# Optimization experiments

Measured on AMD Instinct MI355X. Metric: run time of the kernel, lower is better.

## Reference

```python
import jax, jax.numpy as jnp
import numpy as np

DECAY = 0.99
EPS = 1e-05


def setup_inputs() -> dict:
    key = jax.random.key(0)
    k1, k2 = jax.random.split(key)
    B, C, H, W = 16, 64, 32, 32
    K = 8192
    z_e = jax.random.normal(k1, (B, C, H, W), dtype=jnp.float32)
    embedding = jax.random.normal(k2, (K, C), dtype=jnp.float32)
    cluster_size = jnp.zeros((K,), dtype=jnp.float32)
    embedding_avg = embedding  # initialized as a clone of the codebook
    return {"z_e": z_e, "embedding": embedding, "cluster_size": cluster_size,
            "embedding_avg": embedding_avg}


def reference(z_e, embedding, cluster_size, embedding_avg):
    B, C, H, W = z_e.shape
    K = embedding.shape[0]
    # [N, C] tokens
    z_flat = jnp.transpose(z_e, (0, 2, 3, 1)).reshape(-1, C)
    d = ((z_flat * z_flat).sum(-1, keepdims=True)
         - 2.0 * (z_flat @ embedding.T)
         + (embedding * embedding).sum(-1))
    indices = jnp.argmin(d, axis=1)  # [N] int
    z_q_flat = embedding[indices]    # [N, C]
    z_q = jnp.transpose(z_q_flat.reshape(B, H, W, C), (0, 3, 1, 2))
    # EMA codebook update (training path); one-hot matmuls expressed as segment sums
    counts = jax.ops.segment_sum(jnp.ones(z_flat.shape[0], dtype=z_flat.dtype),
                                 indices, num_segments=K)            # encodings.sum(0)
    dw = jax.ops.segment_sum(z_flat, indices, num_segments=K)        # encodings.T @ z_flat
    new_cluster_size = DECAY * cluster_size + (1.0 - DECAY) * counts
    new_embedding_avg = DECAY * embedding_avg + (1.0 - DECAY) * dw
    n = new_cluster_size.sum()
    cs = (new_cluster_size + EPS) / (n + K * EPS) * n
    new_embedding = new_embedding_avg / cs[:, None]
    # straight-through estimator
    z_q_st = z_e + jax.lax.stop_gradient(z_q - z_e)
    return (z_q_st, indices.reshape(B, H * W), z_q,
            new_embedding, new_cluster_size, new_embedding_avg)
```

## Files before the change

kernel.cpp:

```cpp
#include <hip/hip_runtime.h>

#define DECAYF 0.99f
#define OMDF   0.01f
#define TAU    3.5e-2f

typedef unsigned int u32;
typedef unsigned long long u64;
typedef __attribute__((ext_vector_type(8))) _Float16 f16x8;
typedef __attribute__((ext_vector_type(4))) float f32x4;

#define EN_OFF     0
#define EFRAG_OFF  32768
#define IDX_OFF    32768
#define BEST1_OFF  2129920
#define BEST2_OFF  4227072
#define CNT_OFF    5275648

__device__ __forceinline__ u64 enc_pair(float s, int idx) {
  u32 u = __float_as_uint(s);
  u = (u & 0x80000000u) ? ~u : (u | 0x80000000u);
  return ((u64)u << 32) | (u32)(~idx);
}
__device__ __forceinline__ float dec_score(u64 e) {
  u32 u = (u32)(e >> 32);
  u = (u & 0x80000000u) ? (u & 0x7fffffffu) : ~u;
  return __uint_as_float(u);
}
__device__ __forceinline__ int dec_idx(u64 e) { return (int)(~(u32)e); }
__device__ __forceinline__ unsigned short f2h(float f) {
  union { _Float16 h; unsigned short u; } v;
  v.h = (_Float16)f;
  return v.u;
}
__device__ __forceinline__ float exact_dot(const float* __restrict__ sx,
                                           const float* __restrict__ emb, int k) {
  const float4* e = (const float4*)(emb + (size_t)k * 64);
  float a = 0.f;
#pragma unroll
  for (int q = 0; q < 16; ++q) {
    float4 v = e[q];
    a = fmaf(sx[4 * q],     v.x, a);
    a = fmaf(sx[4 * q + 1], v.y, a);
    a = fmaf(sx[4 * q + 2], v.z, a);
    a = fmaf(sx[4 * q + 3], v.w, a);
  }
  return a;
}

__global__ __launch_bounds__(256) void k_prep(const float* __restrict__ emb,
                                              const float* __restrict__ cs_in,
                                              const float* __restrict__ avg_in,
                                              const float* __restrict__ z_e,
                                              float* __restrict__ en,
                                              unsigned char* __restrict__ efrag,
                                              unsigned char* __restrict__ zfrag,
                                              float* __restrict__ out4,
                                              float* __restrict__ out5,
                                              float* __restrict__ nsum) {
  __shared__ float warr[4];
  __shared__ float sx[64][129];
  int bid = blockIdx.x;
  int t = threadIdx.x;
  if (bid < 512) {
    int tid = bid * 256 + t;
    int k = tid >> 4, q = tid & 15;
    float4 v = ((const float4*)emb)[tid];
    ushort4 hv;
    hv.x = f2h(v.x); hv.y = f2h(v.y); hv.z = f2h(v.z); hv.w = f2h(v.w);
    size_t off = (size_t)(k >> 4) * 2048 + (size_t)(q >> 3) * 1024
               + (size_t)((q >> 1) & 3) * 256 + (size_t)(k & 15) * 16
               + (size_t)(q & 1) * 8;
    *(ushort4*)(efrag + off) = hv;
    float s = v.x * v.x + v.y * v.y + v.z * v.z + v.w * v.w;
    s += __shfl_xor(s, 1, 16);
    s += __shfl_xor(s, 2, 16);
    s += __shfl_xor(s, 4, 16);
    s += __shfl_xor(s, 8, 16);
    if (q == 0) en[k] = 0.5f * s;
  } else if (bid < 1031) {
    int tid = (bid - 512) * 256 + t;
    if (tid < 131072) {
      float4 v = ((const float4*)avg_in)[tid];
      v.x *= DECAYF; v.y *= DECAYF; v.z *= DECAYF; v.w *= DECAYF;
      ((float4*)out5)[tid] = v;
    }
  } else if (bid == 1031) {
    float s = 0.f;
#pragma unroll
    for (int q = 0; q < 8; ++q) {
      int idx = q * 256 + t;
      float4 v = ((const float4*)cs_in)[idx];
      v.x *= DECAYF; v.y *= DECAYF; v.z *= DECAYF; v.w *= DECAYF;
      ((float4*)out4)[idx] = v;
      s += v.x + v.y + v.z + v.w;
    }
    s += __shfl_xor(s, 1, 64);
    s += __shfl_xor(s, 2, 64);
    s += __shfl_xor(s, 4, 64);
    s += __shfl_xor(s, 8, 64);
    s += __shfl_xor(s, 16, 64);
    s += __shfl_xor(s, 32, 64);
    if ((t & 63) == 0) warr[t >> 6] = s;
    __syncthreads();
    if (t == 0) *nsum = warr[0] + warr[1] + warr[2] + warr[3];
  } else {
    int n0 = (bid - 1032) * 128;
    int b = n0 >> 10, hwb = n0 & 1023;
#pragma unroll
    for (int r = 0; r < 8; ++r) {
      int g = r * 256 + t;
      int c = g >> 5, f4 = g & 31;
      float4 v = *(const float4*)(z_e + ((size_t)b << 16) + ((size_t)c << 10)
                                  + hwb + f4 * 4);
      sx[c][f4 * 4 + 0] = v.x;
      sx[c][f4 * 4 + 1] = v.y;
      sx[c][f4 * 4 + 2] = v.z;
      sx[c][f4 * 4 + 3] = v.w;
    }
    __syncthreads();
#pragma unroll
    for (int r = 0; r < 4; ++r) {
      int id = r * 256 + t;
      int nl = id & 127, k = id >> 7;
      int n = n0 + nl;
      unsigned short u[8];
#pragma unroll
      for (int j = 0; j < 8; ++j) u[j] = f2h(sx[k * 8 + j][nl]);
      size_t off = (size_t)(n >> 4) * 2048 + (size_t)(k >> 2) * 1024
                 + (size_t)(k & 3) * 256 + (size_t)(n & 15) * 16;
      *(ushort4*)(zfrag + off)     = make_ushort4(u[0], u[1], u[2], u[3]);
      *(ushort4*)(zfrag + off + 8) = make_ushort4(u[4], u[5], u[6], u[7]);
    }
  }
}

__global__ __launch_bounds__(256) void k_argmin_mfma(
    const unsigned char* __restrict__ zfrag,
    const unsigned char* __restrict__ efrag,
    const float* __restrict__ en, u64* __restrict__ best1,
    float* __restrict__ best2) {
  alignas(16) __shared__ unsigned char sbuf[2][8192];
  __shared__ float sen[512];
  const int tb = blockIdx.x >> 4;
  const int sl = blockIdx.x & 15;
  const int wave = threadIdx.x >> 6, lane = threadIdx.x & 63;
  const int col = lane & 15, g4 = lane >> 4;
  const int token0 = tb * 128 + wave * 32;
  const int scb = sl << 9;

  if (threadIdx.x < 128)
    ((float4*)sen)[threadIdx.x] = ((const float4*)(en + scb))[threadIdx.x];

  f16x8 a[2][2];
  {
    const unsigned char* zb = zfrag + ((size_t)(tb * 8 + wave * 2)) * 2048
                            + (size_t)g4 * 256 + (size_t)col * 16;
    a[0][0] = *(const f16x8*)(zb);
    a[0][1] = *(const f16x8*)(zb + 1024);
    a[1][0] = *(const f16x8*)(zb + 2048);
    a[1][1] = *(const f16x8*)(zb + 3072);
  }
  float b1[8], b2[8];
#pragma unroll
  for (int r = 0; r < 8; ++r) { b1[r] = -3.0e38f; b2[r] = -3.0e38f; }

  const unsigned char* gbase0 = efrag + (size_t)scb * 128;
  auto stage = [&](int ib, int buf) {
    const unsigned char* g = gbase0 + (size_t)ib * 8192 + (size_t)wave * 2048;
#pragma unroll
    for (int it = 0; it < 2; ++it) {
      __builtin_amdgcn_global_load_lds(
          (const __attribute__((address_space(1))) u32*)(g + it * 1024 + lane * 16),
          (__attribute__((address_space(3))) u32*)(&sbuf[buf][wave * 2048 + it * 1024]),
          16, 0, 0);
    }
  };
  stage(0, 0);
  for (int ib = 0; ib < 8; ++ib) {
    __syncthreads();
    if (ib < 7) stage(ib + 1, (ib + 1) & 1);
    const unsigned char* sb0 = &sbuf[ib & 1][0];
#pragma unroll
    for (int ct = 0; ct < 4; ++ct) {
      const int t = ib * 4 + ct;
      const float negen = -sen[t * 16 + col];
      f16x8 bf0 = *(const f16x8*)(sb0 + ct * 2048 + lane * 16);
      f16x8 bf1 = *(const f16x8*)(sb0 + ct * 2048 + 1024 + lane * 16);
      f32x4 acc0, acc1;
#pragma unroll
      for (int r = 0; r < 4; ++r) { acc0[r] = negen; acc1[r] = negen; }
      acc0 = __builtin_amdgcn_mfma_f32_16x16x32_f16(a[0][0], bf0, acc0, 0, 0, 0);
      acc0 = __builtin_amdgcn_mfma_f32_16x16x32_f16(a[0][1], bf1, acc0, 0, 0, 0);
      acc1 = __builtin_amdgcn_mfma_f32_16x16x32_f16(a[1][0], bf0, acc1, 0, 0, 0);
      acc1 = __builtin_amdgcn_mfma_f32_16x16x32_f16(a[1][1], bf1, acc1, 0, 0, 0);
      const u32 emb6 = (u32)(63 - t);
#pragma unroll
      for (int r = 0; r < 4; ++r) {
        float f0 = __uint_as_float((__float_as_uint(acc0[r]) & 0xFFFFFFC0u) | emb6);
        b2[r] = __builtin_amdgcn_fmed3f(f0, b1[r], b2[r]);
        b1[r] = fmaxf(b1[r], f0);
        float f1 = __uint_as_float((__float_as_uint(acc1[r]) & 0xFFFFFFC0u) | emb6);
        b2[4 + r] = __builtin_amdgcn_fmed3f(f1, b1[4 + r], b2[4 + r]);
        b1[4 + r] = fmaxf(b1[4 + r], f1);
      }
    }
  }
  int mi[8];
#pragma unroll
  for (int r = 0; r < 8; ++r) mi[r] = col;
#pragma unroll
  for (int st = 1; st < 16; st <<= 1) {
#pragma unroll
    for (int r = 0; r < 8; ++r) {
      float ob1 = __shfl_xor(b1[r], st, 64);
      float ob2 = __shfl_xor(b2[r], st, 64);
      int omi = __shfl_xor(mi[r], st, 64);
      bool ogt = ob1 > b1[r];
      b2[r] = fmaxf(fminf(b1[r], ob1), fmaxf(b2[r], ob2));
      mi[r] = ogt ? omi : mi[r];
      b1[r] = fmaxf(b1[r], ob1);
    }
  }
  if (col == 0) {
#pragma unroll
    for (int r = 0; r < 8; ++r) {
      int tt = r >> 2, rr = r & 3;
      int token = token0 + tt * 16 + g4 * 4 + rr;
      int t = 63 - (int)(__float_as_uint(b1[r]) & 63u);
      int gcode = scb + t * 16 + mi[r];
      best1[(size_t)sl * 16384 + token] = enc_pair(b1[r], gcode);
      best2[(size_t)sl * 16384 + token] = b2[r];
    }
  }
}

__global__ __launch_bounds__(256) void k_resfix(const float* __restrict__ z_e,
                                                const float* __restrict__ emb,
                                                const float* __restrict__ en,
                                                const u64* __restrict__ best1,
                                                const float* __restrict__ best2,
                                                int* __restrict__ idxa) {
  __shared__ float sxr[64];
  __shared__ int flist[64];
  __shared__ float fth[64];
  __shared__ int nflag;
  __shared__ u32 fmask;
  __shared__ u64 red;
  int t = threadIdx.x;
  int n0 = blockIdx.x * 64;
  if (t == 0) nflag = 0;
  __syncthreads();
  if (t < 64) {
    int n = n0 + t;
    u64 e[16];
#pragma unroll
    for (int s = 0; s < 16; ++s) e[s] = best1[(size_t)s * 16384 + n];
    u64 top = e[0];
#pragma unroll
    for (int s = 1; s < 16; ++s) top = e[s] > top ? e[s] : top;
    float second = -3.0e38f;
#pragma unroll
    for (int s = 0; s < 16; ++s)
      second = fmaxf(second, best2[(size_t)s * 16384 + n]);
#pragma unroll
    for (int s = 0; s < 16; ++s)
      if (e[s] != top) second = fmaxf(second, dec_score(e[s]));
    idxa[n] = dec_idx(top);
    if (dec_score(top) - second < TAU) {
      int p = atomicAdd(&nflag, 1);
      flist[p] = n;
      fth[p] = dec_score(top);
    }
  }
  __syncthreads();
  int nf = nflag;
  for (int i = 0; i < nf; ++i) {
    int n = flist[i];
    float theta = fth[i] - TAU;
    if (t == 0) { fmask = 0; red = 0ull; }
    if (t < 64) {
      sxr[t] = z_e[((size_t)(n >> 10) << 16) + ((size_t)t << 10) + (n & 1023)];
    }
    __syncthreads();
    u64 myb = 0ull;
    if (t < 16) {
      u64 es = best1[(size_t)t * 16384 + n];
      if (best2[(size_t)t * 16384 + n] >= theta) atomicOr(&fmask, 1u << t);
      if (dec_score(es) >= theta) {
        int k = dec_idx(es);
        float a = exact_dot(sxr, emb, k) - en[k];
        myb = enc_pair(a, k);
      }
    }
    __syncthreads();
    u32 fm = fmask;
    while (fm) {
      int s = __ffs(fm) - 1;
      fm &= fm - 1;
      int k0 = (s << 9) + t;
      float a0 = exact_dot(sxr, emb, k0)       - en[k0];
      float a1 = exact_dot(sxr, emb, k0 + 256) - en[k0 + 256];
      u64 m0 = enc_pair(a0, k0), m1 = enc_pair(a1, k0 + 256);
      u64 mm = m0 > m1 ? m0 : m1;
      myb = mm > myb ? mm : myb;
    }
    if (myb) atomicMax(&red, myb);
    __syncthreads();
    if (t == 0) idxa[n] = dec_idx(red);
    __syncthreads();
  }
}

__global__ __launch_bounds__(256) void k_scatter(const float* __restrict__ z_e,
                                                 const int* __restrict__ idxa,
                                                 float* __restrict__ out4,
                                                 float* __restrict__ out5) {
  __shared__ float sx[64][129];
  int t = threadIdx.x;
  int n0 = blockIdx.x * 128;
  int b = n0 >> 10, hwb = n0 & 1023;
#pragma unroll
  for (int r = 0; r < 8; ++r) {
    int g = r * 256 + t;
    int c = g >> 5, f4 = g & 31;
    float4 v = *(const float4*)(z_e + ((size_t)b << 16) + ((size_t)c << 10)
                                + hwb + f4 * 4);
    sx[c][f4 * 4 + 0] = v.x;
    sx[c][f4 * 4 + 1] = v.y;
    sx[c][f4 * 4 + 2] = v.z;
    sx[c][f4 * 4 + 3] = v.w;
  }
  __syncthreads();
  int wave = t >> 6, lane = t & 63;
#pragma unroll
  for (int i = 0; i < 32; ++i) {
    int tok = wave * 32 + i;
    int idx = idxa[n0 + tok];
    atomicAdd(out5 + (size_t)idx * 64 + lane, OMDF * sx[lane][tok]);
    if (lane == 0) atomicAdd(out4 + idx, OMDF);
  }
}

__global__ __launch_bounds__(256) void k_gather(const float* __restrict__ z_e,
                                                const float* __restrict__ emb,
                                                const int* __restrict__ idxa,
                                                float* __restrict__ out0,
                                                float* __restrict__ out1,
                                                float* __restrict__ out2) {
  int tid = blockIdx.x * 256 + threadIdx.x;
  int hw4 = tid & 255;
  int c   = (tid >> 8) & 63;
  int b   = tid >> 14;
  int n0  = (b << 10) + (hw4 << 2);
  size_t off = ((size_t)b << 16) + ((size_t)c << 10) + ((size_t)hw4 << 2);
  float4 z = *(const float4*)(z_e + off);
  int i0 = idxa[n0], i1 = idxa[n0 + 1], i2 = idxa[n0 + 2], i3 = idxa[n0 + 3];
  float4 q;
  q.x = emb[(size_t)i0 * 64 + c];
  q.y = emb[(size_t)i1 * 64 + c];
  q.z = emb[(size_t)i2 * 64 + c];
  q.w = emb[(size_t)i3 * 64 + c];
  float4 st;
  st.x = z.x + (q.x - z.x);
  st.y = z.y + (q.y - z.y);
  st.z = z.z + (q.z - z.z);
  st.w = z.w + (q.w - z.w);
  *(float4*)(out2 + off) = q;
  *(float4*)(out0 + off) = st;
  if (c == 0) {
    float4 f = make_float4((float)i0, (float)i1, (float)i2, (float)i3);
    *(float4*)(out1 + n0) = f;
  }
}

__global__ __launch_bounds__(256) void k_final(const float* __restrict__ out4,
                                               const float* __restrict__ out5,
                                               const float* __restrict__ nsum,
                                               float* __restrict__ out3) {
  int tid = blockIdx.x * 256 + threadIdx.x;
  int k = tid >> 4;
  double nn  = (double)*nsum + 163.84;
  double ncs = (double)out4[k];
  double cs  = (ncs + 1e-5) / (nn + 8192.0 * 1e-5) * nn;
  float inv  = (float)(1.0 / cs);
  float4 v = ((const float4*)out5)[tid];
  v.x *= inv; v.y *= inv; v.z *= inv; v.w *= inv;
  ((float4*)out3)[tid] = v;
}

extern "C" void kernel_launch(void* const* d_in, const int* in_sizes, int n_in,
                              void* d_out, int out_size, void* d_ws, size_t ws_size,
                              hipStream_t stream) {
  const float* z_e    = (const float*)d_in[0];
  const float* emb    = (const float*)d_in[1];
  const float* cs_in  = (const float*)d_in[2];
  const float* avg_in = (const float*)d_in[3];

  float* out  = (float*)d_out;
  float* out0 = out;
  float* out1 = out0 + 1048576;
  float* out2 = out1 + 16384;
  float* out3 = out2 + 1048576;
  float* out4 = out3 + 524288;
  float* out5 = out4 + 8192;

  char* ws = (char*)d_ws;
  float* en            = (float*)(ws + EN_OFF);
  unsigned char* efrag = (unsigned char*)(ws + EFRAG_OFF);
  u64* best1           = (u64*)(ws + BEST1_OFF);
  float* best2         = (float*)(ws + BEST2_OFF);
  int* idxa            = (int*)(ws + IDX_OFF);
  float* nsum          = (float*)(ws + CNT_OFF + 4);
  unsigned char* zfrag = (unsigned char*)out0;

  k_prep       <<<1160, 256, 0, stream>>>(emb, cs_in, avg_in, z_e, en, efrag,
                                          zfrag, out4, out5, nsum);
  k_argmin_mfma<<<2048, 256, 0, stream>>>(zfrag, efrag, en, best1, best2);
  k_resfix     <<<256,  256, 0, stream>>>(z_e, emb, en, best1, best2, idxa);
  k_scatter    <<<128,  256, 0, stream>>>(z_e, idxa, out4, out5);
  k_gather     <<<1024, 256, 0, stream>>>(z_e, emb, idxa, out0, out1, out2);
  k_final      <<<512,  256, 0, stream>>>(out4, out5, nsum, out3);
}
```

Before: 151.5 us.

## Replace atomic scatter with counting-sort segment sums; retile argmin to 64 tokens

The float-atomic scatter of token vectors into the codebook average is replaced by a histogram, a prefix-scan kernel and a fill kernel that build per-code token lists. The gather kernel then sums each code's tokens directly, and the final kernel folds in the counts. Separately, the MFMA argmin kernel is retiled to 64 tokens by 1024 codes per block with 8 code slices instead of 16, which halves the partial-result traffic read by the fixup kernel. The cost is two extra launches, a single-block scan, and uncoalesced per-token reads of z_e in the segment sums.

```diff
diff --git a/kernel.cpp b/kernel.cpp
--- a/kernel.cpp
+++ b/kernel.cpp
@@ -12,9 +12,13 @@
 #define EN_OFF     0
 #define EFRAG_OFF  32768
 #define IDX_OFF    32768
+#define CNT8K_OFF  1081344
+#define OFFS_OFF   1114112
+#define FILLP_OFF  1146880
+#define TOKL_OFF   1179648
 #define BEST1_OFF  2129920
-#define BEST2_OFF  4227072
-#define CNT_OFF    5275648
+#define BEST2_OFF  3178496
+#define NSUM_OFF   3702784
 
 __device__ __forceinline__ u64 enc_pair(float s, int idx) {
   u32 u = __float_as_uint(s);
@@ -56,7 +60,8 @@
                                               unsigned char* __restrict__ zfrag,
                                               float* __restrict__ out4,
                                               float* __restrict__ out5,
-                                              float* __restrict__ nsum) {
+                                              float* __restrict__ nsum,
+                                              int* __restrict__ cnt8k) {
   __shared__ float warr[4];
   __shared__ float sx[64][129];
   int bid = blockIdx.x;
@@ -93,6 +98,7 @@
       v.x *= DECAYF; v.y *= DECAYF; v.z *= DECAYF; v.w *= DECAYF;
       ((float4*)out4)[idx] = v;
       s += v.x + v.y + v.z + v.w;
+      ((int4*)cnt8k)[idx] = make_int4(0, 0, 0, 0);
     }
     s += __shfl_xor(s, 1, 64);
     s += __shfl_xor(s, 2, 64);
@@ -140,29 +146,26 @@
     const float* __restrict__ en, u64* __restrict__ best1,
     float* __restrict__ best2) {
   alignas(16) __shared__ unsigned char sbuf[2][8192];
-  __shared__ float sen[512];
-  const int tb = blockIdx.x >> 4;
-  const int sl = blockIdx.x & 15;
+  __shared__ float sen[1024];
+  const int tb = blockIdx.x >> 3;
+  const int sl = blockIdx.x & 7;
   const int wave = threadIdx.x >> 6, lane = threadIdx.x & 63;
   const int col = lane & 15, g4 = lane >> 4;
-  const int token0 = tb * 128 + wave * 32;
-  const int scb = sl << 9;
-
-  if (threadIdx.x < 128)
-    ((float4*)sen)[threadIdx.x] = ((const float4*)(en + scb))[threadIdx.x];
-
-  f16x8 a[2][2];
+  const int token0 = tb * 64 + wave * 16;
+  const int scb = sl << 10;
+
+  ((float4*)sen)[threadIdx.x] = ((const float4*)(en + scb))[threadIdx.x];
+
+  f16x8 a0, a1;
   {
-    const unsigned char* zb = zfrag + ((size_t)(tb * 8 + wave * 2)) * 2048
+    const unsigned char* zb = zfrag + ((size_t)(tb * 4 + wave)) * 2048
                             + (size_t)g4 * 256 + (size_t)col * 16;
-    a[0][0] = *(const f16x8*)(zb);
-    a[0][1] = *(const f16x8*)(zb + 1024);
-    a[1][0] = *(const f16x8*)(zb + 2048);
-    a[1][1] = *(const f16x8*)(zb + 3072);
-  }
-  float b1[8], b2[8];
-#pragma unroll
-  for (int r = 0; r < 8; ++r) { b1[r] = -3.0e38f; b2[r] = -3.0e38f; }
+    a0 = *(const f16x8*)(zb);
+    a1 = *(const f16x8*)(zb + 1024);
+  }
+  float b1[4], b2[4];
+#pragma unroll
+  for (int r = 0; r < 4; ++r) { b1[r] = -3.0e38f; b2[r] = -3.0e38f; }
 
   const unsigned char* gbase0 = efrag + (size_t)scb * 128;
   auto stage = [&](int ib, int buf) {
@@ -176,9 +179,9 @@
     }
   };
   stage(0, 0);
-  for (int ib = 0; ib < 8; ++ib) {
-    __syncthreads();
-    if (ib < 7) stage(ib + 1, (ib + 1) & 1);
+  for (int ib = 0; ib < 16; ++ib) {
+    __syncthreads();
+    if (ib < 15) stage(ib + 1, (ib + 1) & 1);
     const unsigned char* sb0 = &sbuf[ib & 1][0];
 #pragma unroll
     for (int ct = 0; ct < 4; ++ct) {
@@ -186,32 +189,27 @@
       const float negen = -sen[t * 16 + col];
       f16x8 bf0 = *(const f16x8*)(sb0 + ct * 2048 + lane * 16);
       f16x8 bf1 = *(const f16x8*)(sb0 + ct * 2048 + 1024 + lane * 16);
-      f32x4 acc0, acc1;
-#pragma unroll
-      for (int r = 0; r < 4; ++r) { acc0[r] = negen; acc1[r] = negen; }
-      acc0 = __builtin_amdgcn_mfma_f32_16x16x32_f16(a[0][0], bf0, acc0, 0, 0, 0);
-      acc0 = __builtin_amdgcn_mfma_f32_16x16x32_f16(a[0][1], bf1, acc0, 0, 0, 0);
-      acc1 = __builtin_amdgcn_mfma_f32_16x16x32_f16(a[1][0], bf0, acc1, 0, 0, 0);
-      acc1 = __builtin_amdgcn_mfma_f32_16x16x32_f16(a[1][1], bf1, acc1, 0, 0, 0);
+      f32x4 acc;
+#pragma unroll
+      for (int r = 0; r < 4; ++r) acc[r] = negen;
+      acc = __builtin_amdgcn_mfma_f32_16x16x32_f16(a0, bf0, acc, 0, 0, 0);
+      acc = __builtin_amdgcn_mfma_f32_16x16x32_f16(a1, bf1, acc, 0, 0, 0);
       const u32 emb6 = (u32)(63 - t);
 #pragma unroll
       for (int r = 0; r < 4; ++r) {
-        float f0 = __uint_as_float((__float_as_uint(acc0[r]) & 0xFFFFFFC0u) | emb6);
+        float f0 = __uint_as_float((__float_as_uint(acc[r]) & 0xFFFFFFC0u) | emb6);
         b2[r] = __builtin_amdgcn_fmed3f(f0, b1[r], b2[r]);
         b1[r] = fmaxf(b1[r], f0);
-        float f1 = __uint_as_float((__float_as_uint(acc1[r]) & 0xFFFFFFC0u) | emb6);
-        b2[4 + r] = __builtin_amdgcn_fmed3f(f1, b1[4 + r], b2[4 + r]);
-        b1[4 + r] = fmaxf(b1[4 + r], f1);
       }
     }
   }
-  int mi[8];
-#pragma unroll
-  for (int r = 0; r < 8; ++r) mi[r] = col;
+  int mi[4];
+#pragma unroll
+  for (int r = 0; r < 4; ++r) mi[r] = col;
 #pragma unroll
   for (int st = 1; st < 16; st <<= 1) {
 #pragma unroll
-    for (int r = 0; r < 8; ++r) {
+    for (int r = 0; r < 4; ++r) {
       float ob1 = __shfl_xor(b1[r], st, 64);
       float ob2 = __shfl_xor(b2[r], st, 64);
       int omi = __shfl_xor(mi[r], st, 64);
@@ -223,9 +221,8 @@
   }
   if (col == 0) {
 #pragma unroll
-    for (int r = 0; r < 8; ++r) {
-      int tt = r >> 2, rr = r & 3;
-      int token = token0 + tt * 16 + g4 * 4 + rr;
+    for (int r = 0; r < 4; ++r) {
+      int token = token0 + g4 * 4 + r;
       int t = 63 - (int)(__float_as_uint(b1[r]) & 63u);
       int gcode = scb + t * 16 + mi[r];
       best1[(size_t)sl * 16384 + token] = enc_pair(b1[r], gcode);
@@ -239,8 +236,10 @@
                                                 const float* __restrict__ en,
                                                 const u64* __restrict__ best1,
                                                 const float* __restrict__ best2,
-                                                int* __restrict__ idxa) {
+                                                int* __restrict__ idxa,
+                                                int* __restrict__ cnt8k) {
   __shared__ float sxr[64];
+  __shared__ int sidx[64];
   __shared__ int flist[64];
   __shared__ float fth[64];
   __shared__ int nflag;
@@ -252,20 +251,21 @@
   __syncthreads();
   if (t < 64) {
     int n = n0 + t;
-    u64 e[16];
-#pragma unroll
-    for (int s = 0; s < 16; ++s) e[s] = best1[(size_t)s * 16384 + n];
+    u64 e[8];
+#pragma unroll
+    for (int s = 0; s < 8; ++s) e[s] = best1[(size_t)s * 16384 + n];
     u64 top = e[0];
 #pragma unroll
-    for (int s = 1; s < 16; ++s) top = e[s] > top ? e[s] : top;
+    for (int s = 1; s < 8; ++s) top = e[s] > top ? e[s] : top;
     float second = -3.0e38f;
 #pragma unroll
-    for (int s = 0; s < 16; ++s)
+    for (int s = 0; s < 8; ++s)
       second = fmaxf(second, best2[(size_t)s * 16384 + n]);
 #pragma unroll
-    for (int s = 0; s < 16; ++s)
+    for (int s = 0; s < 8; ++s)
       if (e[s] != top) second = fmaxf(second, dec_score(e[s]));
     idxa[n] = dec_idx(top);
+    sidx[t] = dec_idx(top);
     if (dec_score(top) - second < TAU) {
       int p = atomicAdd(&nflag, 1);
       flist[p] = n;
@@ -283,7 +283,7 @@
     }
     __syncthreads();
     u64 myb = 0ull;
-    if (t < 16) {
+    if (t < 8) {
       u64 es = best1[(size_t)t * 16384 + n];
       if (best2[(size_t)t * 16384 + n] >= theta) atomicOr(&fmask, 1u << t);
       if (dec_score(es) >= theta) {
@@ -297,95 +297,138 @@
     while (fm) {
       int s = __ffs(fm) - 1;
       fm &= fm - 1;
-      int k0 = (s << 9) + t;
+      int k0 = (s << 10) + t;
       float a0 = exact_dot(sxr, emb, k0)       - en[k0];
       float a1 = exact_dot(sxr, emb, k0 + 256) - en[k0 + 256];
-      u64 m0 = enc_pair(a0, k0), m1 = enc_pair(a1, k0 + 256);
-      u64 mm = m0 > m1 ? m0 : m1;
+      float a2 = exact_dot(sxr, emb, k0 + 512) - en[k0 + 512];
+      float a3 = exact_dot(sxr, emb, k0 + 768) - en[k0 + 768];
+      u64 m0 = enc_pair(a0, k0),       m1 = enc_pair(a1, k0 + 256);
+      u64 m2 = enc_pair(a2, k0 + 512), m3 = enc_pair(a3, k0 + 768);
+      u64 ma = m0 > m1 ? m0 : m1, mb = m2 > m3 ? m2 : m3;
+      u64 mm = ma > mb ? ma : mb;
       myb = mm > myb ? mm : myb;
     }
     if (myb) atomicMax(&red, myb);
     __syncthreads();
-    if (t == 0) idxa[n] = dec_idx(red);
-    __syncthreads();
-  }
-}
-
-__global__ __launch_bounds__(256) void k_scatter(const float* __restrict__ z_e,
-                                                 const int* __restrict__ idxa,
-                                                 float* __restrict__ out4,
-                                                 float* __restrict__ out5) {
-  __shared__ float sx[64][129];
+    if (t == 0) {
+      idxa[n] = dec_idx(red);
+      sidx[n - n0] = dec_idx(red);
+    }
+    __syncthreads();
+  }
+  if (t < 64) atomicAdd(&cnt8k[sidx[t]], 1);
+}
+
+__global__ __launch_bounds__(256) void k_scan(const int* __restrict__ cnt8k,
+                                              int* __restrict__ offs,
+                                              int* __restrict__ fillp) {
+  __shared__ int part[256];
   int t = threadIdx.x;
-  int n0 = blockIdx.x * 128;
-  int b = n0 >> 10, hwb = n0 & 1023;
-#pragma unroll
-  for (int r = 0; r < 8; ++r) {
-    int g = r * 256 + t;
-    int c = g >> 5, f4 = g & 31;
-    float4 v = *(const float4*)(z_e + ((size_t)b << 16) + ((size_t)c << 10)
-                                + hwb + f4 * 4);
-    sx[c][f4 * 4 + 0] = v.x;
-    sx[c][f4 * 4 + 1] = v.y;
-    sx[c][f4 * 4 + 2] = v.z;
-    sx[c][f4 * 4 + 3] = v.w;
-  }
+  int loc[32];
+  int s = 0;
+#pragma unroll
+  for (int i = 0; i < 32; ++i) {
+    loc[i] = s;
+    s += cnt8k[t * 32 + i];
+  }
+  part[t] = s;
   __syncthreads();
-  int wave = t >> 6, lane = t & 63;
+  for (int st = 1; st < 256; st <<= 1) {
+    int add = (t >= st) ? part[t - st] : 0;
+    __syncthreads();
+    part[t] += add;
+    __syncthreads();
+  }
+  int base = part[t] - s;
 #pragma unroll
   for (int i = 0; i < 32; ++i) {
-    int tok = wave * 32 + i;
-    int idx = idxa[n0 + tok];
-    atomicAdd(out5 + (size_t)idx * 64 + lane, OMDF * sx[lane][tok]);
-    if (lane == 0) atomicAdd(out4 + idx, OMDF);
-  }
+    int o = base + loc[i];
+    offs[t * 32 + i]  = o;
+    fillp[t * 32 + i] = o;
+  }
+}
+
+__global__ __launch_bounds__(256) void k_fill(const int* __restrict__ idxa,
+                                              int* __restrict__ fillp,
+                                              int* __restrict__ tokl) {
+  int n = blockIdx.x * 256 + threadIdx.x;
+  int idx = idxa[n];
+  int pos = atomicAdd(&fillp[idx], 1);
+  tokl[pos] = n;
 }
 
 __global__ __launch_bounds__(256) void k_gather(const float* __restrict__ z_e,
                                                 const float* __restrict__ emb,
                                                 const int* __restrict__ idxa,
+                                                const int* __restrict__ cnt8k,
+                                                const int* __restrict__ offs,
+                                                const int* __restrict__ tokl,
                                                 float* __restrict__ out0,
                                                 float* __restrict__ out1,
-                                                float* __restrict__ out2) {
+                                                float* __restrict__ out2,
+                                                float* __restrict__ out5) {
   int tid = blockIdx.x * 256 + threadIdx.x;
-  int hw4 = tid & 255;
-  int c   = (tid >> 8) & 63;
-  int b   = tid >> 14;
-  int n0  = (b << 10) + (hw4 << 2);
-  size_t off = ((size_t)b << 16) + ((size_t)c << 10) + ((size_t)hw4 << 2);
-  float4 z = *(const float4*)(z_e + off);
-  int i0 = idxa[n0], i1 = idxa[n0 + 1], i2 = idxa[n0 + 2], i3 = idxa[n0 + 3];
-  float4 q;
-  q.x = emb[(size_t)i0 * 64 + c];
-  q.y = emb[(size_t)i1 * 64 + c];
-  q.z = emb[(size_t)i2 * 64 + c];
-  q.w = emb[(size_t)i3 * 64 + c];
-  float4 st;
-  st.x = z.x + (q.x - z.x);
-  st.y = z.y + (q.y - z.y);
-  st.z = z.z + (q.z - z.z);
-  st.w = z.w + (q.w - z.w);
-  *(float4*)(out2 + off) = q;
-  *(float4*)(out0 + off) = st;
-  if (c == 0) {
-    float4 f = make_float4((float)i0, (float)i1, (float)i2, (float)i3);
-    *(float4*)(out1 + n0) = f;
-  }
-}
-
-__global__ __launch_bounds__(256) void k_final(const float* __restrict__ out4,
+  {
+    int hw4 = tid & 255;
+    int c   = (tid >> 8) & 63;
+    int b   = tid >> 14;
+    int n0  = (b << 10) + (hw4 << 2);
+    size_t off = ((size_t)b << 16) + ((size_t)c << 10) + ((size_t)hw4 << 2);
+    float4 z = *(const float4*)(z_e + off);
+    int i0 = idxa[n0], i1 = idxa[n0 + 1], i2 = idxa[n0 + 2], i3 = idxa[n0 + 3];
+    float4 q;
+    q.x = emb[(size_t)i0 * 64 + c];
+    q.y = emb[(size_t)i1 * 64 + c];
+    q.z = emb[(size_t)i2 * 64 + c];
+    q.w = emb[(size_t)i3 * 64 + c];
+    float4 st;
+    st.x = z.x + (q.x - z.x);
+    st.y = z.y + (q.y - z.y);
+    st.z = z.z + (q.z - z.z);
+    st.w = z.w + (q.w - z.w);
+    *(float4*)(out2 + off) = q;
+    *(float4*)(out0 + off) = st;
+    if (c == 0) {
+      float4 f = make_float4((float)i0, (float)i1, (float)i2, (float)i3);
+      *(float4*)(out1 + n0) = f;
+    }
+  }
+  {
+    int wv = blockIdx.x * 4 + (threadIdx.x >> 6);
+    int lane = threadIdx.x & 63;
+#pragma unroll
+    for (int rep = 0; rep < 2; ++rep) {
+      int k = wv * 2 + rep;
+      int cnt = cnt8k[k];
+      int o = offs[k];
+      float sum = 0.f;
+      for (int j = 0; j < cnt; ++j) {
+        int n = tokl[o + j];
+        sum += z_e[((size_t)(n >> 10) << 16) + ((size_t)lane << 10) + (n & 1023)];
+      }
+      if (cnt > 0) {
+        size_t oi = (size_t)k * 64 + lane;
+        out5[oi] = fmaf(OMDF, sum, out5[oi]);
+      }
+    }
+  }
+}
+
+__global__ __launch_bounds__(256) void k_final(float* __restrict__ out4,
                                                const float* __restrict__ out5,
                                                const float* __restrict__ nsum,
+                                               const int* __restrict__ cnt8k,
                                                float* __restrict__ out3) {
   int tid = blockIdx.x * 256 + threadIdx.x;
   int k = tid >> 4;
+  float ncsf = fmaf(OMDF, (float)cnt8k[k], out4[k]);
   double nn  = (double)*nsum + 163.84;
-  double ncs = (double)out4[k];
-  double cs  = (ncs + 1e-5) / (nn + 8192.0 * 1e-5) * nn;
+  double cs  = ((double)ncsf + 1e-5) / (nn + 8192.0 * 1e-5) * nn;
   float inv  = (float)(1.0 / cs);
   float4 v = ((const float4*)out5)[tid];
   v.x *= inv; v.y *= inv; v.z *= inv; v.w *= inv;
   ((float4*)out3)[tid] = v;
+  if ((tid & 15) == 0) out4[k] = ncsf;
 }
 
 extern "C" void kernel_launch(void* const* d_in, const int* in_sizes, int n_in,
@@ -407,17 +450,23 @@
   char* ws = (char*)d_ws;
   float* en            = (float*)(ws + EN_OFF);
   unsigned char* efrag = (unsigned char*)(ws + EFRAG_OFF);
+  int* idxa            = (int*)(ws + IDX_OFF);
+  int* cnt8k           = (int*)(ws + CNT8K_OFF);
+  int* offs            = (int*)(ws + OFFS_OFF);
+  int* fillp           = (int*)(ws + FILLP_OFF);
+  int* tokl            = (int*)(ws + TOKL_OFF);
   u64* best1           = (u64*)(ws + BEST1_OFF);
   float* best2         = (float*)(ws + BEST2_OFF);
-  int* idxa            = (int*)(ws + IDX_OFF);
-  float* nsum          = (float*)(ws + CNT_OFF + 4);
+  float* nsum          = (float*)(ws + NSUM_OFF);
   unsigned char* zfrag = (unsigned char*)out0;
 
   k_prep       <<<1160, 256, 0, stream>>>(emb, cs_in, avg_in, z_e, en, efrag,
-                                          zfrag, out4, out5, nsum);
+                                          zfrag, out4, out5, nsum, cnt8k);
   k_argmin_mfma<<<2048, 256, 0, stream>>>(zfrag, efrag, en, best1, best2);
-  k_resfix     <<<256,  256, 0, stream>>>(z_e, emb, en, best1, best2, idxa);
-  k_scatter    <<<128,  256, 0, stream>>>(z_e, idxa, out4, out5);
-  k_gather     <<<1024, 256, 0, stream>>>(z_e, emb, idxa, out0, out1, out2);
-  k_final      <<<512,  256, 0, stream>>>(out4, out5, nsum, out3);
-}
+  k_resfix     <<<256,  256, 0, stream>>>(z_e, emb, en, best1, best2, idxa, cnt8k);
+  k_scan       <<<1,    256, 0, stream>>>(cnt8k, offs, fillp);
+  k_fill       <<<64,   256, 0, stream>>>(idxa, fillp, tokl);
+  k_gather     <<<1024, 256, 0, stream>>>(z_e, emb, idxa, cnt8k, offs, tokl,
+                                          out0, out1, out2, out5);
+  k_final      <<<512,  256, 0, stream>>>(out4, out5, nsum, cnt8k, out3);
+}
```

New measurement: 180.8 us. +19.4%, slower.
